# Optimization experiments

Measured on AMD Instinct MI355X. Metric: run time of the kernel, lower is better.

Reference implementation:

```python
import jax, jax.numpy as jnp
import numpy as np

N, H, G = 500_000, 128, 1024

def setup_inputs() -> dict:
    key = jax.random.key(0)
    k1, k2, k3, k4 = jax.random.split(key, 4)
    x = jax.random.normal(k1, (N, H), dtype=jnp.float32)
    batch = jnp.sort(jax.random.randint(k2, (N,), 0, G)).astype(jnp.int64)
    gate_w = jax.random.normal(k3, (H, 1), dtype=jnp.float32) * (1.0 / np.sqrt(H))
    gate_b = jnp.zeros((1,), dtype=jnp.float32)
    combine_w = jax.random.normal(k4, (3 * H, H), dtype=jnp.float32) * (1.0 / np.sqrt(3 * H))
    combine_b = jnp.zeros((H,), dtype=jnp.float32)
    return {"x": x, "batch": batch, "gate_w": gate_w, "gate_b": gate_b,
            "combine_w": combine_w, "combine_b": combine_b, "num_graphs": G}

def reference(x, batch, gate_w, gate_b, combine_w, combine_b, num_graphs):
    # --- GlobalAttention pool: segment softmax over gate scores, weighted sum ---
    gate = (x @ gate_w + gate_b)[:, 0]                                  # [N]
    gmax = jax.ops.segment_max(gate, batch, num_segments=num_graphs)    # [G]
    gmax = jnp.where(jnp.isfinite(gmax), gmax, 0.0)                     # guard empty segments
    e = jnp.exp(gate - gmax[batch])                                     # [N]
    denom = jax.ops.segment_sum(e, batch, num_segments=num_graphs)      # [G]
    alpha = e / jnp.maximum(denom, 1e-16)[batch]                        # [N]
    att = jax.ops.segment_sum(alpha[:, None] * x, batch, num_segments=num_graphs)  # [G,H]

    # --- global_mean_pool ---
    s = jax.ops.segment_sum(x, batch, num_segments=num_graphs)          # [G,H]
    cnt = jax.ops.segment_sum(jnp.ones((x.shape[0],), x.dtype), batch, num_segments=num_graphs)
    mean = s / jnp.maximum(cnt, 1.0)[:, None]

    # --- global_max_pool ---
    mx = jax.ops.segment_max(x, batch, num_segments=num_graphs)         # [G,H]
    mx = jnp.where(jnp.isfinite(mx), mx, 0.0)

    combined = jnp.concatenate([att, mean, mx], axis=1)                 # [G,3H]
    return combined @ combine_w + combine_b                             # [G,H]
```

## Files before the change

kernel.cpp:

```cpp
#include <hip/hip_runtime.h>
#include <math.h>

#define H 128
#define CHUNK 256

__device__ __forceinline__ unsigned fenc(float v) {
    unsigned u = __float_as_uint(v);
    return (u & 0x80000000u) ? ~u : (u | 0x80000000u);
}
__device__ __forceinline__ float fdec(unsigned u) {
    return __uint_as_float((u & 0x80000000u) ? (u ^ 0x80000000u) : ~u);
}

__global__ __launch_bounds__(256, 4)
void accum_kernel(const float* __restrict__ x,
                  const int*   __restrict__ batch,
                  const float* __restrict__ gate_w,
                  const float* __restrict__ gate_b,
                  float*    __restrict__ ws_att,
                  float*    __restrict__ ws_sum,
                  unsigned* __restrict__ ws_mx,
                  float*    __restrict__ ws_den,
                  unsigned* __restrict__ ws_cnt,
                  int N)
{
    const int t    = threadIdx.x;
    const int grp  = t >> 5;
    const int lane = t & 31;
    const int r0   = blockIdx.x * CHUNK;
    if (r0 >= N) return;
    const int len  = min(CHUNK, N - r0);

    __shared__ int s_b[CHUNK];
    __shared__ unsigned long long s_mask[4];
    __shared__ float s_att[8][H];
    __shared__ float s_sum[8][H];
    __shared__ float s_mx[8][H];
    __shared__ float s_d[8];

    if (t < len) s_b[t] = batch[r0 + t];
    __syncthreads();
    bool flag = (t > 0) && (t < len) && (s_b[t] != s_b[t - 1]);
    unsigned long long bm = __ballot(flag);
    if ((t & 63) == 0) s_mask[t >> 6] = bm;
    __syncthreads();

    const float4 gw = ((const float4*)gate_w)[lane];
    const float  gb = gate_b[0];
    const float4* xv = (const float4*)x;

    int s = 0;
    while (s < len) {
        const int g = s_b[s];

        int e = len;
        {
            int w = (s + 1) >> 6;
            if (w < 4) {
                unsigned long long mm = s_mask[w] & (~0ULL << ((s + 1) & 63));
                while (true) {
                    if (mm) { e = (w << 6) + __ffsll(mm) - 1; break; }
                    if (++w >= 4) break;
                    mm = s_mask[w];
                }
            }
        }
        const int aS = r0 + s, aE = r0 + e;

        float  d   = 0.0f;
        float4 att = make_float4(0.f, 0.f, 0.f, 0.f);
        float4 sum = make_float4(0.f, 0.f, 0.f, 0.f);
        float4 mx  = make_float4(-INFINITY, -INFINITY, -INFINITY, -INFINITY);

        int  rA = aS + grp;
        bool v0 = rA     < aE;
        bool v1 = rA + 8 < aE;
        float4 c0 = make_float4(0.f, 0.f, 0.f, 0.f);
        float4 c1 = make_float4(0.f, 0.f, 0.f, 0.f);
        if (v0) c0 = xv[(size_t)rA * 32 + lane];
        if (v1) c1 = xv[(size_t)(rA + 8) * 32 + lane];

        while (v0) {
            const int rN = rA + 16;
            bool n0v = rN     < aE;
            bool n1v = rN + 8 < aE;
            float4 n0 = make_float4(0.f, 0.f, 0.f, 0.f);
            float4 n1 = make_float4(0.f, 0.f, 0.f, 0.f);
            if (n0v) n0 = xv[(size_t)rN * 32 + lane];
            if (n1v) n1 = xv[(size_t)(rN + 8) * 32 + lane];

            float p0 = c0.x*gw.x + c0.y*gw.y + c0.z*gw.z + c0.w*gw.w;
            float p1 = c1.x*gw.x + c1.y*gw.y + c1.z*gw.z + c1.w*gw.w;
            p0 += __shfl_xor(p0, 1);  p1 += __shfl_xor(p1, 1);
            p0 += __shfl_xor(p0, 2);  p1 += __shfl_xor(p1, 2);
            p0 += __shfl_xor(p0, 4);  p1 += __shfl_xor(p1, 4);
            p0 += __shfl_xor(p0, 8);  p1 += __shfl_xor(p1, 8);
            p0 += __shfl_xor(p0, 16); p1 += __shfl_xor(p1, 16);

            float e0 = __expf(p0 + gb);
            float e1 = v1 ? __expf(p1 + gb) : 0.0f;

            d += e0 + e1;
            att.x += e0*c0.x + e1*c1.x;
            att.y += e0*c0.y + e1*c1.y;
            att.z += e0*c0.z + e1*c1.z;
            att.w += e0*c0.w + e1*c1.w;
            sum.x += c0.x + c1.x;
            sum.y += c0.y + c1.y;
            sum.z += c0.z + c1.z;
            sum.w += c0.w + c1.w;
            mx.x = fmaxf(mx.x, c0.x); mx.y = fmaxf(mx.y, c0.y);
            mx.z = fmaxf(mx.z, c0.z); mx.w = fmaxf(mx.w, c0.w);
            if (v1) {
                mx.x = fmaxf(mx.x, c1.x); mx.y = fmaxf(mx.y, c1.y);
                mx.z = fmaxf(mx.z, c1.z); mx.w = fmaxf(mx.w, c1.w);
            }
            rA = rN; c0 = n0; c1 = n1; v0 = n0v; v1 = n1v;
        }

        ((float4*)s_att[grp])[lane] = att;
        ((float4*)s_sum[grp])[lane] = sum;
        ((float4*)s_mx[grp])[lane]  = mx;
        if (lane == 0) s_d[grp] = d;
        __syncthreads();

        if (t < H) {
            float a = 0.f, sm = 0.f, mxf = -INFINITY;
            #pragma unroll
            for (int k = 0; k < 8; k++) {
                a  += s_att[k][t];
                sm += s_sum[k][t];
                mxf = fmaxf(mxf, s_mx[k][t]);
            }
            atomicAdd(&ws_att[(size_t)g * H + t], a);
            atomicAdd(&ws_sum[(size_t)g * H + t], sm);
            atomicMax(&ws_mx[(size_t)g * H + t], fenc(mxf));
        } else if (t == H) {
            float D = 0.f;
            #pragma unroll
            for (int k = 0; k < 8; k++) D += s_d[k];
            atomicAdd(&ws_den[g], D);
            atomicAdd(&ws_cnt[g], (unsigned)(e - s));
        }
        __syncthreads();
        s = e;
    }
}

__global__ __launch_bounds__(256, 4)
void finish_kernel(const float*    __restrict__ ws_att,
                   const float*    __restrict__ ws_sum,
                   const unsigned* __restrict__ ws_mx,
                   const float*    __restrict__ ws_den,
                   const unsigned* __restrict__ ws_cnt,
                   const float*    __restrict__ combine_w,
                   const float*    __restrict__ combine_b,
                   float*          __restrict__ out)
{
    const int g = blockIdx.x;
    const int t = threadIdx.x;

    __shared__ float s_comb[3 * H];
    __shared__ float s_part[H];

    if (t < H) {
        unsigned cnt = ws_cnt[g];
        float o_att, o_mean, o_mx;
        if (cnt > 0) {
            float D = ws_den[g];
            o_att  = ws_att[(size_t)g * H + t] / fmaxf(D, 1e-16f);
            o_mean = ws_sum[(size_t)g * H + t] / (float)cnt;
            o_mx   = fdec(ws_mx[(size_t)g * H + t]);
        } else {
            o_att = 0.f; o_mean = 0.f; o_mx = 0.f;
        }
        s_comb[t]         = o_att;
        s_comb[H + t]     = o_mean;
        s_comb[2 * H + t] = o_mx;
    }
    __syncthreads();

    const int j    = t & (H - 1);
    const int half = t >> 7;
    const int k0   = half * 192;
    float acc = 0.f;
    #pragma unroll 8
    for (int k = k0; k < k0 + 192; k++)
        acc += s_comb[k] * combine_w[k * H + j];
    if (half == 0) s_part[j] = acc;
    __syncthreads();
    if (half == 1)
        out[(size_t)g * H + j] = acc + s_part[j] + combine_b[j];
}

extern "C" void kernel_launch(void* const* d_in, const int* in_sizes, int n_in,
                              void* d_out, int out_size, void* d_ws, size_t ws_size,
                              hipStream_t stream) {
    const float* x         = (const float*)d_in[0];
    const int*   batch     = (const int*)d_in[1];
    const float* gate_w    = (const float*)d_in[2];
    const float* gate_b    = (const float*)d_in[3];
    const float* combine_w = (const float*)d_in[4];
    const float* combine_b = (const float*)d_in[5];
    float* out = (float*)d_out;

    const int N = in_sizes[0] / H;
    const int G = out_size / H;

    float*    ws_att = (float*)d_ws;
    float*    ws_sum = ws_att + (size_t)G * H;
    unsigned* ws_mx  = (unsigned*)(ws_sum + (size_t)G * H);
    float*    ws_den = (float*)(ws_mx + (size_t)G * H);
    unsigned* ws_cnt = (unsigned*)(ws_den + G);
    const size_t ws_bytes = ((size_t)3 * G * H + 2 * (size_t)G) * sizeof(float);

    hipMemsetAsync(d_ws, 0, ws_bytes, stream);

    const int nblk = (N + CHUNK - 1) / CHUNK;
    accum_kernel<<<nblk, 256, 0, stream>>>(x, batch, gate_w, gate_b,
                                           ws_att, ws_sum, ws_mx, ws_den, ws_cnt, N);
    finish_kernel<<<G, 256, 0, stream>>>(ws_att, ws_sum, ws_mx, ws_den, ws_cnt,
                                         combine_w, combine_b, out);
}
```

Measured before the change: 381.8 us.

## Double rows per block and unroll accumulation loop to four rows per wave

Each block now covers 512 rows instead of 256, which halves the block count and reduces how often a segment is split across blocks and flushed with global atomics. The inner loop now handles four rows per 32-lane group per iteration and prefetches four rows ahead, putting more loads in flight to hide memory latency. The cost is higher register pressure, which could reduce occupancy under the launch bounds, and a longer serial loop per block.

```diff
diff --git a/kernel.cpp b/kernel.cpp
--- a/kernel.cpp
+++ b/kernel.cpp
@@ -2,7 +2,8 @@
 #include <math.h>
 
 #define H 128
-#define CHUNK 256
+#define CHUNK 512
+#define NW (CHUNK / 64)
 
 __device__ __forceinline__ unsigned fenc(float v) {
     unsigned u = __float_as_uint(v);
@@ -32,17 +33,25 @@
     const int len  = min(CHUNK, N - r0);
 
     __shared__ int s_b[CHUNK];
-    __shared__ unsigned long long s_mask[4];
+    __shared__ unsigned long long s_mask[NW];
     __shared__ float s_att[8][H];
     __shared__ float s_sum[8][H];
     __shared__ float s_mx[8][H];
     __shared__ float s_d[8];
 
-    if (t < len) s_b[t] = batch[r0 + t];
-    __syncthreads();
-    bool flag = (t > 0) && (t < len) && (s_b[t] != s_b[t - 1]);
-    unsigned long long bm = __ballot(flag);
-    if ((t & 63) == 0) s_mask[t >> 6] = bm;
+    #pragma unroll
+    for (int h = 0; h < CHUNK / 256; h++) {
+        int idx = h * 256 + t;
+        if (idx < len) s_b[idx] = batch[r0 + idx];
+    }
+    __syncthreads();
+    #pragma unroll
+    for (int h = 0; h < CHUNK / 256; h++) {
+        int idx = h * 256 + t;
+        bool flag = (idx > 0) && (idx < len) && (s_b[idx] != s_b[idx - 1]);
+        unsigned long long bm = __ballot(flag);
+        if ((t & 63) == 0) s_mask[h * 4 + (t >> 6)] = bm;
+    }
     __syncthreads();
 
     const float4 gw = ((const float4*)gate_w)[lane];
@@ -56,11 +65,11 @@
         int e = len;
         {
             int w = (s + 1) >> 6;
-            if (w < 4) {
+            if (w < NW) {
                 unsigned long long mm = s_mask[w] & (~0ULL << ((s + 1) & 63));
                 while (true) {
                     if (mm) { e = (w << 6) + __ffsll(mm) - 1; break; }
-                    if (++w >= 4) break;
+                    if (++w >= NW) break;
                     mm = s_mask[w];
                 }
             }
@@ -73,49 +82,75 @@
         float4 mx  = make_float4(-INFINITY, -INFINITY, -INFINITY, -INFINITY);
 
         int  rA = aS + grp;
-        bool v0 = rA     < aE;
-        bool v1 = rA + 8 < aE;
-        float4 c0 = make_float4(0.f, 0.f, 0.f, 0.f);
-        float4 c1 = make_float4(0.f, 0.f, 0.f, 0.f);
+        bool v0 = rA      < aE;
+        bool v1 = rA + 8  < aE;
+        bool v2 = rA + 16 < aE;
+        bool v3 = rA + 24 < aE;
+        float4 z  = make_float4(0.f, 0.f, 0.f, 0.f);
+        float4 c0 = z, c1 = z, c2 = z, c3 = z;
         if (v0) c0 = xv[(size_t)rA * 32 + lane];
         if (v1) c1 = xv[(size_t)(rA + 8) * 32 + lane];
+        if (v2) c2 = xv[(size_t)(rA + 16) * 32 + lane];
+        if (v3) c3 = xv[(size_t)(rA + 24) * 32 + lane];
 
         while (v0) {
-            const int rN = rA + 16;
-            bool n0v = rN     < aE;
-            bool n1v = rN + 8 < aE;
-            float4 n0 = make_float4(0.f, 0.f, 0.f, 0.f);
-            float4 n1 = make_float4(0.f, 0.f, 0.f, 0.f);
-            if (n0v) n0 = xv[(size_t)rN * 32 + lane];
-            if (n1v) n1 = xv[(size_t)(rN + 8) * 32 + lane];
+            const int rN = rA + 32;
+            bool m0 = rN      < aE;
+            bool m1 = rN + 8  < aE;
+            bool m2 = rN + 16 < aE;
+            bool m3 = rN + 24 < aE;
+            float4 n0 = z, n1 = z, n2 = z, n3 = z;
+            if (m0) n0 = xv[(size_t)rN * 32 + lane];
+            if (m1) n1 = xv[(size_t)(rN + 8) * 32 + lane];
+            if (m2) n2 = xv[(size_t)(rN + 16) * 32 + lane];
+            if (m3) n3 = xv[(size_t)(rN + 24) * 32 + lane];
 
             float p0 = c0.x*gw.x + c0.y*gw.y + c0.z*gw.z + c0.w*gw.w;
             float p1 = c1.x*gw.x + c1.y*gw.y + c1.z*gw.z + c1.w*gw.w;
+            float p2 = c2.x*gw.x + c2.y*gw.y + c2.z*gw.z + c2.w*gw.w;
+            float p3 = c3.x*gw.x + c3.y*gw.y + c3.z*gw.z + c3.w*gw.w;
             p0 += __shfl_xor(p0, 1);  p1 += __shfl_xor(p1, 1);
+            p2 += __shfl_xor(p2, 1);  p3 += __shfl_xor(p3, 1);
             p0 += __shfl_xor(p0, 2);  p1 += __shfl_xor(p1, 2);
+            p2 += __shfl_xor(p2, 2);  p3 += __shfl_xor(p3, 2);
             p0 += __shfl_xor(p0, 4);  p1 += __shfl_xor(p1, 4);
+            p2 += __shfl_xor(p2, 4);  p3 += __shfl_xor(p3, 4);
             p0 += __shfl_xor(p0, 8);  p1 += __shfl_xor(p1, 8);
+            p2 += __shfl_xor(p2, 8);  p3 += __shfl_xor(p3, 8);
             p0 += __shfl_xor(p0, 16); p1 += __shfl_xor(p1, 16);
+            p2 += __shfl_xor(p2, 16); p3 += __shfl_xor(p3, 16);
 
             float e0 = __expf(p0 + gb);
             float e1 = v1 ? __expf(p1 + gb) : 0.0f;
-
-            d += e0 + e1;
-            att.x += e0*c0.x + e1*c1.x;
-            att.y += e0*c0.y + e1*c1.y;
-            att.z += e0*c0.z + e1*c1.z;
-            att.w += e0*c0.w + e1*c1.w;
-            sum.x += c0.x + c1.x;
-            sum.y += c0.y + c1.y;
-            sum.z += c0.z + c1.z;
-            sum.w += c0.w + c1.w;
+            float e2 = v2 ? __expf(p2 + gb) : 0.0f;
+            float e3 = v3 ? __expf(p3 + gb) : 0.0f;
+
+            d += (e0 + e1) + (e2 + e3);
+            att.x += e0*c0.x + e1*c1.x + e2*c2.x + e3*c3.x;
+            att.y += e0*c0.y + e1*c1.y + e2*c2.y + e3*c3.y;
+            att.z += e0*c0.z + e1*c1.z + e2*c2.z + e3*c3.z;
+            att.w += e0*c0.w + e1*c1.w + e2*c2.w + e3*c3.w;
+            sum.x += (c0.x + c1.x) + (c2.x + c3.x);
+            sum.y += (c0.y + c1.y) + (c2.y + c3.y);
+            sum.z += (c0.z + c1.z) + (c2.z + c3.z);
+            sum.w += (c0.w + c1.w) + (c2.w + c3.w);
             mx.x = fmaxf(mx.x, c0.x); mx.y = fmaxf(mx.y, c0.y);
             mx.z = fmaxf(mx.z, c0.z); mx.w = fmaxf(mx.w, c0.w);
             if (v1) {
                 mx.x = fmaxf(mx.x, c1.x); mx.y = fmaxf(mx.y, c1.y);
                 mx.z = fmaxf(mx.z, c1.z); mx.w = fmaxf(mx.w, c1.w);
             }
-            rA = rN; c0 = n0; c1 = n1; v0 = n0v; v1 = n1v;
+            if (v2) {
+                mx.x = fmaxf(mx.x, c2.x); mx.y = fmaxf(mx.y, c2.y);
+                mx.z = fmaxf(mx.z, c2.z); mx.w = fmaxf(mx.w, c2.w);
+            }
+            if (v3) {
+                mx.x = fmaxf(mx.x, c3.x); mx.y = fmaxf(mx.y, c3.y);
+                mx.z = fmaxf(mx.z, c3.z); mx.w = fmaxf(mx.w, c3.w);
+            }
+            rA = rN;
+            c0 = n0; c1 = n1; c2 = n2; c3 = n3;
+            v0 = m0; v1 = m1; v2 = m2; v3 = m3;
         }
 
         ((float4*)s_att[grp])[lane] = att;
```

New measurement: 376.6 us. About the same (-1.4%).
